# Kernel tuning notes

Measured on AMD Instinct MI355X. Metric: run time of the kernel, lower is better.

The kernel has to match this reference:

```python
import jax, jax.numpy as jnp
import numpy as np

B, K, H, W = 8, 32, 480, 480
N, D = 576, 1024
NUM_CLASSES, CLS_DIM, OUT = 150, 64, 256
IN_DIM = D + CLS_DIM + 5


def setup_inputs() -> dict:
    key = jax.random.key(0)
    ks = jax.random.split(key, 8)
    return {
        "feature_map": jax.random.normal(ks[0], (B, N, D), dtype=jnp.float32),
        "masks": jax.random.randint(ks[1], (B, K, H, W), 0, 2, dtype=jnp.int32),
        "class_ids": jax.random.randint(ks[2], (B, K), 0, NUM_CLASSES, dtype=jnp.int64),
        "embed_table": jax.random.normal(ks[3], (NUM_CLASSES, CLS_DIM), dtype=jnp.float32),
        "W1": jax.random.normal(ks[4], (IN_DIM, OUT), dtype=jnp.float32) * 0.02,
        "b1": jnp.zeros((OUT,), dtype=jnp.float32),
        "ln_g": jnp.ones((OUT,), dtype=jnp.float32),
        "ln_b": jnp.zeros((OUT,), dtype=jnp.float32),
        "W2": jax.random.normal(ks[5], (OUT, OUT), dtype=jnp.float32) * 0.02,
        "b2": jnp.zeros((OUT,), dtype=jnp.float32),
    }


def _geom_feats(m):
    # m: [B,K,H,W] float binary masks -> [B,K,5] (cx, cy, area_norm, bbox_w, bbox_h)
    dt = m.dtype
    area = m.sum((-2, -1))                      # [B,K]
    safe = jnp.maximum(area, 1.0)
    xs = jnp.arange(W, dtype=dt)
    ys = jnp.arange(H, dtype=dt)
    cx = jnp.einsum('bkhw,w->bk', m, xs) / safe / W
    cy = jnp.einsum('bkhw,h->bk', m, ys) / safe / H
    col = m.max(axis=2)                          # [B,K,W] column occupancy
    row = m.max(axis=3)                          # [B,K,H] row occupancy
    x_min = jnp.min(jnp.where(col > 0, xs, float(W)), axis=-1)
    x_max = jnp.max(jnp.where(col > 0, xs, -1.0), axis=-1)
    y_min = jnp.min(jnp.where(row > 0, ys, float(H)), axis=-1)
    y_max = jnp.max(jnp.where(row > 0, ys, -1.0), axis=-1)
    bbox_w = (x_max - x_min + 1.0) / W
    bbox_h = (y_max - y_min + 1.0) / H
    area_norm = area / (H * W)
    geom = jnp.stack([cx, cy, area_norm, bbox_w, bbox_h], axis=-1)  # [B,K,5]
    valid = (area >= 1.0)[..., None]
    return jnp.where(valid, geom, 0.0)


def reference(feature_map, masks, class_ids, embed_table, W1, b1, ln_g, ln_b, W2, b2):
    Hf = Wf = int(round(N ** 0.5))  # 24
    m = (masks > 0).astype(feature_map.dtype)           # [B,K,H,W]
    # nearest-neighbor downsample (PyTorch 'nearest': src = floor(dst*in/out))
    idx_h = (jnp.arange(Hf) * H) // Hf
    idx_w = (jnp.arange(Wf) * W) // Wf
    m_rs = m[:, :, idx_h][:, :, :, idx_w]               # [B,K,Hf,Wf]
    m_flat = m_rs.reshape(B, K, Hf * Wf)                # [B,K,N]
    msum = jnp.clip(m_flat.sum(-1, keepdims=True), 1e-6, None)
    pooled = jnp.einsum('bkn,bnd->bkd', m_flat, feature_map) / msum  # [B,K,D]
    geom = _geom_feats(m)                               # [B,K,5]
    cls_emb = embed_table[class_ids]                    # [B,K,CLS_DIM]
    x = jnp.concatenate([pooled, cls_emb, geom], axis=-1)  # [B,K,IN_DIM]
    h = jax.nn.gelu(x @ W1 + b1, approximate=False)
    mu = h.mean(-1, keepdims=True)
    var = jnp.mean((h - mu) ** 2, axis=-1, keepdims=True)
    hn = (h - mu) * jax.lax.rsqrt(var + 1e-5) * ln_g + ln_b
    return hn @ W2 + b2                                 # [B,K,OUT]
```

## Files before the change

kernel.cpp:

```cpp
#include <hip/hip_runtime.h>
#include <math.h>

#define Bb 8
#define Kk 32
#define Hh 480
#define Ww 480
#define Nn 576
#define Dd 1024
#define CLSD 64
#define OUTD 256
#define INDIM 1093
#define BK 256

typedef int v4i __attribute__((ext_vector_type(4)));

__global__ __launch_bounds__(1024) void kF(const int* __restrict__ masks,
                                           const float* __restrict__ fm,
                                           const int* __restrict__ cids,
                                           const float* __restrict__ emb,
                                           const float* __restrict__ W1,
                                           const float* __restrict__ b1,
                                           const float* __restrict__ lg,
                                           const float* __restrict__ lb,
                                           const float* __restrict__ W2,
                                           const float* __restrict__ b2,
                                           float* __restrict__ out) {
  const int b    = blockIdx.x & 7;
  const int k    = blockIdx.x >> 3;
  const int bk   = b * Kk + k;
  const int t    = threadIdx.x;
  const int lane = t & 63;
  const int w    = t >> 6;

  __shared__ int    actw[4][576];
  __shared__ float4 x4s[256];
  __shared__ float  partial[16 * 256];
  __shared__ float  hrow[256];
  __shared__ float  red_s[4], red_q[4];
  __shared__ float  gmeta[8];
  __shared__ int    gstat[12][7];

  const int* mbase = masks + (size_t)bk * (Hh * Ww);

  if (w < 12) {
    int area = 0, sumx = 0, sumy = 0;
    int minx = Ww, maxx = -1, miny = Hh, maxy = -1;
    const v4i* mp = (const v4i*)mbase;
#pragma unroll 5
    for (int i = 0; i < 75; i++) {
      int q = t + i * 768;
      v4i v = __builtin_nontemporal_load(mp + q);
      int h   = q / 120;
      int rem = q - h * 120;
      int w0  = rem * 4;
      int m0 = v.x > 0, m1 = v.y > 0, m2 = v.z > 0, m3 = v.w > 0;
      int c = m0 + m1 + m2 + m3;
      area += c;
      sumy += h * c;
      sumx += w0 * c + m1 + 2 * m2 + 3 * m3;
      if (c) {
        miny = min(miny, h);
        maxy = max(maxy, h);
        int lo = m0 ? w0 : (m1 ? w0 + 1 : (m2 ? w0 + 2 : w0 + 3));
        int hi = m3 ? w0 + 3 : (m2 ? w0 + 2 : (m1 ? w0 + 1 : w0));
        minx = min(minx, lo);
        maxx = max(maxx, hi);
      }
    }
    for (int off = 32; off; off >>= 1) {
      area += __shfl_down(area, off);
      sumx += __shfl_down(sumx, off);
      sumy += __shfl_down(sumy, off);
      minx = min(minx, __shfl_down(minx, off));
      maxx = max(maxx, __shfl_down(maxx, off));
      miny = min(miny, __shfl_down(miny, off));
      maxy = max(maxy, __shfl_down(maxy, off));
    }
    if (lane == 0) {
      gstat[w][0] = area; gstat[w][1] = sumx; gstat[w][2] = sumy;
      gstat[w][3] = minx; gstat[w][4] = maxx;
      gstat[w][5] = miny; gstat[w][6] = maxy;
    }
  } else {
    const int cw   = w - 12;
    const int base = cw * 64 + lane;

    int mv[9];
#pragma unroll
    for (int r = 0; r < 9; r++) {
      int p = r * 64 + lane;
      int a = p / 24, c = p - a * 24;
      mv[r] = mbase[(a * 20) * Ww + c * 20];
    }
    int na = 0;
    int* actp = actw[cw];
#pragma unroll
    for (int r = 0; r < 9; r++) {
      unsigned long long bal = __ballot(mv[r] > 0);
      int idx = __popcll(bal & ((1ull << lane) - 1));
      if (mv[r] > 0) actp[na + idx] = r * 64 + lane;
      na += __popcll(bal);
    }

    const float4* fmp = (const float4*)fm + (size_t)b * Nn * (Dd / 4);
    float ax = 0.f, ay = 0.f, az = 0.f, aw = 0.f;
    int j = 0;
    for (; j + 4 <= na; j += 4) {
      int n0 = actp[j], n1 = actp[j + 1], n2 = actp[j + 2], n3 = actp[j + 3];
      float4 f0 = fmp[n0 * (Dd / 4) + base];
      float4 f1 = fmp[n1 * (Dd / 4) + base];
      float4 f2 = fmp[n2 * (Dd / 4) + base];
      float4 f3 = fmp[n3 * (Dd / 4) + base];
      ax += f0.x + f1.x + f2.x + f3.x;
      ay += f0.y + f1.y + f2.y + f3.y;
      az += f0.z + f1.z + f2.z + f3.z;
      aw += f0.w + f1.w + f2.w + f3.w;
    }
    for (; j < na; j++) {
      float4 f = fmp[actp[j] * (Dd / 4) + base];
      ax += f.x; ay += f.y; az += f.z; aw += f.w;
    }
    float inv = 1.0f / fmaxf((float)na, 1e-6f);
    float4 xp;
    xp.x = ax * inv; xp.y = ay * inv; xp.z = az * inv; xp.w = aw * inv;
    x4s[base] = xp;

    float4 acc = {0.f, 0.f, 0.f, 0.f};
    const float* W1b = W1 + (size_t)(cw * 256) * OUTD + 4 * lane;
#pragma unroll 2
    for (int g = 0; g < 64; g++) {
      float4 xv = x4s[cw * 64 + g];
      const float* xs = (const float*)&xv;
#pragma unroll
      for (int u = 0; u < 4; u++) {
        float4 w4 = *(const float4*)(W1b + (size_t)(4 * g + u) * OUTD);
        acc.x = fmaf(xs[u], w4.x, acc.x);
        acc.y = fmaf(xs[u], w4.y, acc.y);
        acc.z = fmaf(xs[u], w4.z, acc.z);
        acc.w = fmaf(xs[u], w4.w, acc.w);
      }
    }
    *(float4*)(partial + cw * 256 + 4 * lane) = acc;
  }
  __syncthreads();

  if (t == 0) {
    int area = 0, sumx = 0, sumy = 0;
    int minx = Ww, maxx = -1, miny = Hh, maxy = -1;
#pragma unroll
    for (int i = 0; i < 12; i++) {
      area += gstat[i][0]; sumx += gstat[i][1]; sumy += gstat[i][2];
      minx = min(minx, gstat[i][3]); maxx = max(maxx, gstat[i][4]);
      miny = min(miny, gstat[i][5]); maxy = max(maxy, gstat[i][6]);
    }
    float areaf = (float)area;
    float safe  = fmaxf(areaf, 1.0f);
    float cx = ((float)sumx / safe) * (1.0f / Ww);
    float cy = ((float)sumy / safe) * (1.0f / Hh);
    float an = areaf * (1.0f / (Hh * Ww));
    float bw = (float)(maxx - minx + 1) * (1.0f / Ww);
    float bh = (float)(maxy - miny + 1) * (1.0f / Hh);
    if (area < 1) { cx = 0.f; cy = 0.f; an = 0.f; bw = 0.f; bh = 0.f; }
    gmeta[0] = cx; gmeta[1] = cy; gmeta[2] = an; gmeta[3] = bw; gmeta[4] = bh;
  }
  __syncthreads();

  float hv = 0.f;
  if (t < 256) {
    hv = b1[t] + partial[t] + partial[256 + t] + partial[512 + t] + partial[768 + t];
    const float* et = emb + (size_t)cids[bk] * CLSD;
#pragma unroll 8
    for (int i = 0; i < CLSD; i++)
      hv = fmaf(et[i], W1[(size_t)(Dd + i) * OUTD + t], hv);
#pragma unroll
    for (int jj = 0; jj < 5; jj++)
      hv = fmaf(gmeta[jj], W1[(size_t)(Dd + CLSD + jj) * OUTD + t], hv);
    hv = 0.5f * hv * (1.0f + erff(hv * 0.7071067811865475f));
  }
  {
    float s = hv, q = hv * hv;
    for (int off = 32; off; off >>= 1) {
      s += __shfl_down(s, off);
      q += __shfl_down(q, off);
    }
    if (lane == 0 && w < 4) { red_s[w] = s; red_q[w] = q; }
  }
  __syncthreads();
  if (t < 256) {
    float s = red_s[0] + red_s[1] + red_s[2] + red_s[3];
    float q = red_q[0] + red_q[1] + red_q[2] + red_q[3];
    float mu  = s * (1.0f / OUTD);
    float var = q * (1.0f / OUTD) - mu * mu;
    float ist = 1.0f / sqrtf(var + 1e-5f);
    hrow[t] = (hv - mu) * ist * lg[t] + lb[t];
  }
  __syncthreads();

  {
    float4 acc = {0.f, 0.f, 0.f, 0.f};
#pragma unroll
    for (int i = 0; i < 4; i++) {
      float4 h4 = ((const float4*)hrow)[w * 4 + i];
      const float* hs = (const float*)&h4;
#pragma unroll
      for (int u = 0; u < 4; u++) {
        int kk = w * 16 + i * 4 + u;
        float4 w4 = *(const float4*)(W2 + (size_t)kk * OUTD + 4 * lane);
        acc.x = fmaf(hs[u], w4.x, acc.x);
        acc.y = fmaf(hs[u], w4.y, acc.y);
        acc.z = fmaf(hs[u], w4.z, acc.z);
        acc.w = fmaf(hs[u], w4.w, acc.w);
      }
    }
    *(float4*)(partial + w * 256 + 4 * lane) = acc;
  }
  __syncthreads();

  if (t < 256) {
    float c = b2[t];
#pragma unroll
    for (int ww = 0; ww < 16; ww++) c += partial[ww * 256 + t];
    __builtin_nontemporal_store(c, out + (size_t)bk * OUTD + t);
  }
}

extern "C" void kernel_launch(void* const* d_in, const int* in_sizes, int n_in,
                              void* d_out, int out_size, void* d_ws, size_t ws_size,
                              hipStream_t stream) {
  const float* fm    = (const float*)d_in[0];
  const int*   masks = (const int*)d_in[1];
  const int*   cids  = (const int*)d_in[2];
  const float* emb   = (const float*)d_in[3];
  const float* W1    = (const float*)d_in[4];
  const float* b1    = (const float*)d_in[5];
  const float* lg    = (const float*)d_in[6];
  const float* lb    = (const float*)d_in[7];
  const float* W2    = (const float*)d_in[8];
  const float* b2    = (const float*)d_in[9];
  float* out = (float*)d_out;

  hipLaunchKernelGGL(kF, dim3(BK), dim3(1024), 0, stream, masks, fm, cids, emb,
                     W1, b1, lg, lb, W2, b2, out);
}
```

Measured before the change: 370.0 us.

## Run pooling and W1 GEMV on all 16 waves before the full-block mask scan

Replaces the 12/4 wave specialization with a phased design. All 1024 threads first sample the downsampled mask into a shared byte map, then pool feature rows with 4 row groups, then split the 1024x256 W1 product across 16 waves. After that, all 16 waves scan the full-resolution mask for geometry stats. The goal is to stop 4 waves from serially pooling and running the GEMV while 12 waves stream the mask. In exchange, the work runs in sequential phases with extra barriers, so the mask streaming no longer overlaps the feature/W1 loads.

```diff
diff --git a/kernel.cpp b/kernel.cpp
--- a/kernel.cpp
+++ b/kernel.cpp
@@ -32,41 +32,108 @@
   const int lane = t & 63;
   const int w    = t >> 6;
 
-  __shared__ int    actw[4][576];
+  __shared__ float  partial[16 * 256];
   __shared__ float4 x4s[256];
-  __shared__ float  partial[16 * 256];
   __shared__ float  hrow[256];
   __shared__ float  red_s[4], red_q[4];
   __shared__ float  gmeta[8];
-  __shared__ int    gstat[12][7];
+  __shared__ int    gstat[16][7];
+  __shared__ unsigned char m576[576];
+  __shared__ int    nact;
 
   const int* mbase = masks + (size_t)bk * (Hh * Ww);
 
-  if (w < 12) {
+  if (t == 0) nact = 0;
+  if (t < 576) {
+    int a = t / 24, c = t - a * 24;
+    int mv = mbase[(a * 20) * Ww + c * 20];
+    m576[t] = (mv > 0);
+    unsigned long long bal = __ballot(mv > 0);
+    if (lane == 0) atomicAdd(&nact, __popcll(bal));
+  }
+  __syncthreads();
+  const int na = nact;
+
+  {
+    const int grp  = t >> 8;
+    const int colf = t & 255;
+    const float4* fmp = (const float4*)fm + (size_t)b * Nn * (Dd / 4);
+    float ax = 0.f, ay = 0.f, az = 0.f, aw = 0.f;
+    for (int n = grp; n < Nn; n += 4) {
+      if (m576[n]) {
+        float4 f = fmp[n * (Dd / 4) + colf];
+        ax += f.x; ay += f.y; az += f.z; aw += f.w;
+      }
+    }
+    float4* pools = (float4*)partial;
+    float4 p; p.x = ax; p.y = ay; p.z = az; p.w = aw;
+    pools[grp * 256 + colf] = p;
+  }
+  __syncthreads();
+  if (t < 256) {
+    const float4* pools = (const float4*)partial;
+    float4 p0 = pools[t], p1 = pools[256 + t], p2 = pools[512 + t], p3 = pools[768 + t];
+    float inv = 1.0f / fmaxf((float)na, 1e-6f);
+    float4 xp;
+    xp.x = (p0.x + p1.x + p2.x + p3.x) * inv;
+    xp.y = (p0.y + p1.y + p2.y + p3.y) * inv;
+    xp.z = (p0.z + p1.z + p2.z + p3.z) * inv;
+    xp.w = (p0.w + p1.w + p2.w + p3.w) * inv;
+    x4s[t] = xp;
+  }
+  __syncthreads();
+
+  {
+    float4 acc = {0.f, 0.f, 0.f, 0.f};
+    const float* W1b = W1 + (size_t)(w * 64) * OUTD + 4 * lane;
+#pragma unroll 4
+    for (int g = 0; g < 16; g++) {
+      float4 xv = x4s[w * 16 + g];
+      const float* xs = (const float*)&xv;
+#pragma unroll
+      for (int u = 0; u < 4; u++) {
+        float4 w4 = *(const float4*)(W1b + (size_t)(4 * g + u) * OUTD);
+        acc.x = fmaf(xs[u], w4.x, acc.x);
+        acc.y = fmaf(xs[u], w4.y, acc.y);
+        acc.z = fmaf(xs[u], w4.z, acc.z);
+        acc.w = fmaf(xs[u], w4.w, acc.w);
+      }
+    }
+    *(float4*)(partial + w * 256 + 4 * lane) = acc;
+  }
+
+  {
     int area = 0, sumx = 0, sumy = 0;
     int minx = Ww, maxx = -1, miny = Hh, maxy = -1;
     const v4i* mp = (const v4i*)mbase;
-#pragma unroll 5
-    for (int i = 0; i < 75; i++) {
-      int q = t + i * 768;
-      v4i v = __builtin_nontemporal_load(mp + q);
-      int h   = q / 120;
-      int rem = q - h * 120;
-      int w0  = rem * 4;
-      int m0 = v.x > 0, m1 = v.y > 0, m2 = v.z > 0, m3 = v.w > 0;
-      int c = m0 + m1 + m2 + m3;
-      area += c;
-      sumy += h * c;
-      sumx += w0 * c + m1 + 2 * m2 + 3 * m3;
-      if (c) {
-        miny = min(miny, h);
-        maxy = max(maxy, h);
-        int lo = m0 ? w0 : (m1 ? w0 + 1 : (m2 ? w0 + 2 : w0 + 3));
-        int hi = m3 ? w0 + 3 : (m2 ? w0 + 2 : (m1 ? w0 + 1 : w0));
-        minx = min(minx, lo);
-        maxx = max(maxx, hi);
-      }
-    }
+
+#define SCAN_BODY(qq)                                                   \
+    {                                                                   \
+      int q = (qq);                                                     \
+      v4i v = __builtin_nontemporal_load(mp + q);                       \
+      int h   = q / 120;                                                \
+      int rem = q - h * 120;                                            \
+      int w0  = rem * 4;                                                \
+      int m0 = v.x > 0, m1 = v.y > 0, m2 = v.z > 0, m3 = v.w > 0;       \
+      int c = m0 + m1 + m2 + m3;                                        \
+      area += c;                                                        \
+      sumy += h * c;                                                    \
+      sumx += w0 * c + m1 + 2 * m2 + 3 * m3;                            \
+      if (c) {                                                          \
+        miny = min(miny, h);                                            \
+        maxy = max(maxy, h);                                            \
+        int lo = m0 ? w0 : (m1 ? w0 + 1 : (m2 ? w0 + 2 : w0 + 3));      \
+        int hi = m3 ? w0 + 3 : (m2 ? w0 + 2 : (m1 ? w0 + 1 : w0));      \
+        minx = min(minx, lo);                                           \
+        maxx = max(maxx, hi);                                           \
+      }                                                                 \
+    }
+
+#pragma unroll 4
+    for (int i = 0; i < 56; i++) SCAN_BODY(t + i * 1024)
+    if (t < 256) SCAN_BODY(57344 + t)
+#undef SCAN_BODY
+
     for (int off = 32; off; off >>= 1) {
       area += __shfl_down(area, off);
       sumx += __shfl_down(sumx, off);
@@ -81,66 +148,6 @@
       gstat[w][3] = minx; gstat[w][4] = maxx;
       gstat[w][5] = miny; gstat[w][6] = maxy;
     }
-  } else {
-    const int cw   = w - 12;
-    const int base = cw * 64 + lane;
-
-    int mv[9];
-#pragma unroll
-    for (int r = 0; r < 9; r++) {
-      int p = r * 64 + lane;
-      int a = p / 24, c = p - a * 24;
-      mv[r] = mbase[(a * 20) * Ww + c * 20];
-    }
-    int na = 0;
-    int* actp = actw[cw];
-#pragma unroll
-    for (int r = 0; r < 9; r++) {
-      unsigned long long bal = __ballot(mv[r] > 0);
-      int idx = __popcll(bal & ((1ull << lane) - 1));
-      if (mv[r] > 0) actp[na + idx] = r * 64 + lane;
-      na += __popcll(bal);
-    }
-
-    const float4* fmp = (const float4*)fm + (size_t)b * Nn * (Dd / 4);
-    float ax = 0.f, ay = 0.f, az = 0.f, aw = 0.f;
-    int j = 0;
-    for (; j + 4 <= na; j += 4) {
-      int n0 = actp[j], n1 = actp[j + 1], n2 = actp[j + 2], n3 = actp[j + 3];
-      float4 f0 = fmp[n0 * (Dd / 4) + base];
-      float4 f1 = fmp[n1 * (Dd / 4) + base];
-      float4 f2 = fmp[n2 * (Dd / 4) + base];
-      float4 f3 = fmp[n3 * (Dd / 4) + base];
-      ax += f0.x + f1.x + f2.x + f3.x;
-      ay += f0.y + f1.y + f2.y + f3.y;
-      az += f0.z + f1.z + f2.z + f3.z;
-      aw += f0.w + f1.w + f2.w + f3.w;
-    }
-    for (; j < na; j++) {
-      float4 f = fmp[actp[j] * (Dd / 4) + base];
-      ax += f.x; ay += f.y; az += f.z; aw += f.w;
-    }
-    float inv = 1.0f / fmaxf((float)na, 1e-6f);
-    float4 xp;
-    xp.x = ax * inv; xp.y = ay * inv; xp.z = az * inv; xp.w = aw * inv;
-    x4s[base] = xp;
-
-    float4 acc = {0.f, 0.f, 0.f, 0.f};
-    const float* W1b = W1 + (size_t)(cw * 256) * OUTD + 4 * lane;
-#pragma unroll 2
-    for (int g = 0; g < 64; g++) {
-      float4 xv = x4s[cw * 64 + g];
-      const float* xs = (const float*)&xv;
-#pragma unroll
-      for (int u = 0; u < 4; u++) {
-        float4 w4 = *(const float4*)(W1b + (size_t)(4 * g + u) * OUTD);
-        acc.x = fmaf(xs[u], w4.x, acc.x);
-        acc.y = fmaf(xs[u], w4.y, acc.y);
-        acc.z = fmaf(xs[u], w4.z, acc.z);
-        acc.w = fmaf(xs[u], w4.w, acc.w);
-      }
-    }
-    *(float4*)(partial + cw * 256 + 4 * lane) = acc;
   }
   __syncthreads();
 
@@ -148,7 +155,7 @@
     int area = 0, sumx = 0, sumy = 0;
     int minx = Ww, maxx = -1, miny = Hh, maxy = -1;
 #pragma unroll
-    for (int i = 0; i < 12; i++) {
+    for (int i = 0; i < 16; i++) {
       area += gstat[i][0]; sumx += gstat[i][1]; sumy += gstat[i][2];
       minx = min(minx, gstat[i][3]); maxx = max(maxx, gstat[i][4]);
       miny = min(miny, gstat[i][5]); maxy = max(maxy, gstat[i][6]);
@@ -167,7 +174,9 @@
 
   float hv = 0.f;
   if (t < 256) {
-    hv = b1[t] + partial[t] + partial[256 + t] + partial[512 + t] + partial[768 + t];
+    hv = b1[t];
+#pragma unroll
+    for (int ww = 0; ww < 16; ww++) hv += partial[ww * 256 + t];
     const float* et = emb + (size_t)cids[bk] * CLSD;
 #pragma unroll 8
     for (int i = 0; i < CLSD; i++)
```

New measurement: 376.7 us. No clear change (+1.8%).

## Stream mask tiles into LDS with async global_load_lds pipeline

Applied to the files above, without the earlier changes.

The 12 mask-statistics waves now each own a contiguous 4800-vector slice of the mask. They stream it through an 8-deep ring of LDS slots using `global_load_lds` direct-to-LDS loads, gated by `vmcnt` waits and scheduling barriers, instead of plain nontemporal register loads. The aim is more memory-level parallelism on the dominant mask read, which looks latency-bound with one 1024-thread block per CU. In exchange, static shared arrays move to a roughly 127 KB dynamic LDS allocation, which needs the large LDS of gfx950 and rules out co-resident blocks.

```diff
diff --git a/kernel.cpp b/kernel.cpp
--- a/kernel.cpp
+++ b/kernel.cpp
@@ -9,10 +9,23 @@
 #define Dd 1024
 #define CLSD 64
 #define OUTD 256
-#define INDIM 1093
 #define BK 256
 
 typedef int v4i __attribute__((ext_vector_type(4)));
+
+typedef __attribute__((address_space(1))) const int gas_int;
+typedef __attribute__((address_space(3))) int las_int;
+
+#define OFF_DMA     0
+#define OFF_ACTW    98304
+#define OFF_X4S     107520
+#define OFF_PART    111616
+#define OFF_HROW    128000
+#define OFF_REDS    129024
+#define OFF_REDQ    129040
+#define OFF_GMETA   129056
+#define OFF_GSTAT   129088
+#define SMEM_BYTES  129536
 
 __global__ __launch_bounds__(1024) void kF(const int* __restrict__ masks,
                                            const float* __restrict__ fm,
@@ -32,41 +45,71 @@
   const int lane = t & 63;
   const int w    = t >> 6;
 
-  __shared__ int    actw[4][576];
-  __shared__ float4 x4s[256];
-  __shared__ float  partial[16 * 256];
-  __shared__ float  hrow[256];
-  __shared__ float  red_s[4], red_q[4];
-  __shared__ float  gmeta[8];
-  __shared__ int    gstat[12][7];
+  extern __shared__ char smem[];
+  int*    dma     = (int*)(smem + OFF_DMA);
+  int*    actw    = (int*)(smem + OFF_ACTW);
+  float4* x4s     = (float4*)(smem + OFF_X4S);
+  float*  partial = (float*)(smem + OFF_PART);
+  float*  hrow    = (float*)(smem + OFF_HROW);
+  float*  red_s   = (float*)(smem + OFF_REDS);
+  float*  red_q   = (float*)(smem + OFF_REDQ);
+  float*  gmeta   = (float*)(smem + OFF_GMETA);
+  int*    gstat   = (int*)(smem + OFF_GSTAT);
 
   const int* mbase = masks + (size_t)bk * (Hh * Ww);
 
   if (w < 12) {
+    const int g0   = w * 4800;
+    int* dmaW      = dma + w * 2048;
+    const char* gsrc0 = (const char*)mbase + (size_t)(g0 + lane) * 16;
+
+#define ISSUE(cc)                                                        \
+    __builtin_amdgcn_global_load_lds(                                    \
+        (gas_int*)(gsrc0 + (size_t)(cc) * 1024),                         \
+        (las_int*)(dmaW + (((cc) & 7) << 8)), 16, 0, 0)
+
+#define STAT_BODY(cc)                                                    \
+    {                                                                    \
+      v4i v = *(const v4i*)(dmaW + (((cc) & 7) << 8) + lane * 4);        \
+      int g    = g0 + (cc) * 64 + lane;                                  \
+      int h    = g / 120;                          \
+      int rem  = g - h * 120;                                            \
+      int w0   = rem * 4;                                                \
+      int m0 = v.x > 0, m1 = v.y > 0, m2 = v.z > 0, m3 = v.w > 0;        \
+      int cnt = m0 + m1 + m2 + m3;                                       \
+      area += cnt;                                                       \
+      sumy += h * cnt;                                                   \
+      sumx += w0 * cnt + m1 + 2 * m2 + 3 * m3;                           \
+      if (cnt) {                                                         \
+        miny = min(miny, h);                                             \
+        maxy = max(maxy, h);                                             \
+        int lo = m0 ? w0 : (m1 ? w0 + 1 : (m2 ? w0 + 2 : w0 + 3));       \
+        int hi = m3 ? w0 + 3 : (m2 ? w0 + 2 : (m1 ? w0 + 1 : w0));       \
+        minx = min(minx, lo);                                            \
+        maxx = max(maxx, hi);                                            \
+      }                                                                  \
+    }
+
+#pragma unroll
+    for (int s = 0; s < 8; s++) ISSUE(s);
+
     int area = 0, sumx = 0, sumy = 0;
     int minx = Ww, maxx = -1, miny = Hh, maxy = -1;
-    const v4i* mp = (const v4i*)mbase;
-#pragma unroll 5
-    for (int i = 0; i < 75; i++) {
-      int q = t + i * 768;
-      v4i v = __builtin_nontemporal_load(mp + q);
-      int h   = q / 120;
-      int rem = q - h * 120;
-      int w0  = rem * 4;
-      int m0 = v.x > 0, m1 = v.y > 0, m2 = v.z > 0, m3 = v.w > 0;
-      int c = m0 + m1 + m2 + m3;
-      area += c;
-      sumy += h * c;
-      sumx += w0 * c + m1 + 2 * m2 + 3 * m3;
-      if (c) {
-        miny = min(miny, h);
-        maxy = max(maxy, h);
-        int lo = m0 ? w0 : (m1 ? w0 + 1 : (m2 ? w0 + 2 : w0 + 3));
-        int hi = m3 ? w0 + 3 : (m2 ? w0 + 2 : (m1 ? w0 + 1 : w0));
-        minx = min(minx, lo);
-        maxx = max(maxx, hi);
-      }
-    }
+
+    for (int c = 0; c < 67; c++) {
+      asm volatile("s_waitcnt vmcnt(7)" ::: "memory");
+      __builtin_amdgcn_sched_barrier(0);
+      STAT_BODY(c)
+      __builtin_amdgcn_sched_barrier(0);
+      ISSUE(c + 8);
+    }
+    asm volatile("s_waitcnt vmcnt(0)" ::: "memory");
+    __builtin_amdgcn_sched_barrier(0);
+#pragma unroll
+    for (int c = 67; c < 75; c++) STAT_BODY(c)
+#undef ISSUE
+#undef STAT_BODY
+
     for (int off = 32; off; off >>= 1) {
       area += __shfl_down(area, off);
       sumx += __shfl_down(sumx, off);
@@ -77,9 +120,9 @@
       maxy = max(maxy, __shfl_down(maxy, off));
     }
     if (lane == 0) {
-      gstat[w][0] = area; gstat[w][1] = sumx; gstat[w][2] = sumy;
-      gstat[w][3] = minx; gstat[w][4] = maxx;
-      gstat[w][5] = miny; gstat[w][6] = maxy;
+      gstat[w * 7 + 0] = area; gstat[w * 7 + 1] = sumx; gstat[w * 7 + 2] = sumy;
+      gstat[w * 7 + 3] = minx; gstat[w * 7 + 4] = maxx;
+      gstat[w * 7 + 5] = miny; gstat[w * 7 + 6] = maxy;
     }
   } else {
     const int cw   = w - 12;
@@ -93,7 +136,7 @@
       mv[r] = mbase[(a * 20) * Ww + c * 20];
     }
     int na = 0;
-    int* actp = actw[cw];
+    int* actp = actw + cw * 576;
 #pragma unroll
     for (int r = 0; r < 9; r++) {
       unsigned long long bal = __ballot(mv[r] > 0);
@@ -149,9 +192,9 @@
     int minx = Ww, maxx = -1, miny = Hh, maxy = -1;
 #pragma unroll
     for (int i = 0; i < 12; i++) {
-      area += gstat[i][0]; sumx += gstat[i][1]; sumy += gstat[i][2];
-      minx = min(minx, gstat[i][3]); maxx = max(maxx, gstat[i][4]);
-      miny = min(miny, gstat[i][5]); maxy = max(maxy, gstat[i][6]);
+      area += gstat[i * 7 + 0]; sumx += gstat[i * 7 + 1]; sumy += gstat[i * 7 + 2];
+      minx = min(minx, gstat[i * 7 + 3]); maxx = max(maxx, gstat[i * 7 + 4]);
+      miny = min(miny, gstat[i * 7 + 5]); maxy = max(maxy, gstat[i * 7 + 6]);
     }
     float areaf = (float)area;
     float safe  = fmaxf(areaf, 1.0f);
@@ -239,6 +282,6 @@
   const float* b2    = (const float*)d_in[9];
   float* out = (float*)d_out;
 
-  hipLaunchKernelGGL(kF, dim3(BK), dim3(1024), 0, stream, masks, fm, cids, emb,
-                     W1, b1, lg, lb, W2, b2, out);
+  hipLaunchKernelGGL(kF, dim3(BK), dim3(1024), SMEM_BYTES, stream, masks, fm,
+                     cids, emb, W1, b1, lg, lb, W2, b2, out);
 }
```

Result: slower. 389.9 us (+5.4%).
